# Kernel optimization log

Hardware: AMD Instinct MI355X
Metric: run time of the kernel (lower is better)

Reference implementation:

```python
import jax, jax.numpy as jnp
import numpy as np

BN_EPS = 1e-5

def setup_inputs() -> dict:
    key = jax.random.key(0)
    ks = jax.random.split(key, 7)
    B, D, A = 16384, 768, 51
    s = 1.0 / np.sqrt(D)
    return {
        "x": jax.random.normal(ks[0], (B, D), dtype=jnp.float32),
        "W_embed": jax.random.uniform(ks[1], (D, D), minval=-s, maxval=s, dtype=jnp.float32),
        "b_embed": jax.random.uniform(ks[2], (D,), minval=-s, maxval=s, dtype=jnp.float32),
        "W_attr": jax.random.uniform(ks[3], (A, D), minval=-s, maxval=s, dtype=jnp.float32),  # stacked per-attribute (dim->1) heads
        "b_attr": jax.random.uniform(ks[4], (A,), minval=-s, maxval=s, dtype=jnp.float32),
        "gamma": jnp.ones((A,), dtype=jnp.float32),
        "beta": jnp.zeros((A,), dtype=jnp.float32),
    }

def reference(x, W_embed, b_embed, W_attr, b_attr, gamma, beta):
    # word_embed: Linear(dim, dim)
    h = x @ W_embed.T + b_embed                      # [B, D]
    # fused per-attribute heads: cat of attr_num (dim->1) linears == one (dim->attr_num) matmul
    logits = h @ W_attr.T + b_attr                    # [B, A]
    # BatchNorm1d (training mode: batch statistics, biased variance)
    mean = jnp.mean(logits, axis=0)
    var = jnp.var(logits, axis=0)
    y = (logits - mean) * jax.lax.rsqrt(var + BN_EPS) * gamma + beta
    return y
```

## Files before the change

### kernel.cpp

```cpp
#include <hip/hip_runtime.h>
#include <hip/hip_bf16.h>

typedef _Float16 halfx8 __attribute__((ext_vector_type(8)));
typedef _Float16 halfx4 __attribute__((ext_vector_type(4)));
typedef float floatx4 __attribute__((ext_vector_type(4)));

#define GLOBAL_AS __attribute__((address_space(1)))
#define LDS_AS __attribute__((address_space(3)))

__device__ __forceinline__ void async_copy_16(const _Float16* g, _Float16* l) {
    __builtin_amdgcn_global_load_lds((GLOBAL_AS void*)g, (LDS_AS void*)l, 16, 0, 0);
}

#define PM 16384
#define PD 768
#define PA 51
#define PA_PAD 64


__global__ void convert_all_kernel(const float* __restrict__ x, const float* __restrict__ We,
                                   const float* __restrict__ Wa,
                                   _Float16* __restrict__ x16, _Float16* __restrict__ we16,
                                   _Float16* __restrict__ wa16, float* __restrict__ stats) {
    int b = blockIdx.x, t = threadIdx.x;
    if (b < 12288) {
        int idx = b * 256 + t;
        float4 v = ((const float4*)x)[idx];
        halfx4 h;
        h[0] = (_Float16)v.x; h[1] = (_Float16)v.y; h[2] = (_Float16)v.z; h[3] = (_Float16)v.w;
        *(halfx4*)(x16 + (size_t)idx * 4) = h;
    } else if (b < 12288 + 576) {
        int idx = (b - 12288) * 256 + t;
        float4 v = ((const float4*)We)[idx];
        halfx4 h;
        h[0] = (_Float16)v.x; h[1] = (_Float16)v.y; h[2] = (_Float16)v.z; h[3] = (_Float16)v.w;
        *(halfx4*)(we16 + (size_t)idx * 4) = h;
    } else if (b < 12288 + 624) {
        int j = (b - 12288 - 576) * 256 + t;
        halfx4 h;
        if (j < (PA * PD) / 4) {
            float4 v = ((const float4*)Wa)[j];
            h[0] = (_Float16)v.x; h[1] = (_Float16)v.y; h[2] = (_Float16)v.z; h[3] = (_Float16)v.w;
        } else {
            h[0] = (_Float16)0.f; h[1] = (_Float16)0.f; h[2] = (_Float16)0.f; h[3] = (_Float16)0.f;
        }
        *(halfx4*)(wa16 + (size_t)j * 4) = h;
    } else {
        if (t < 128) stats[t] = 0.f;
    }
}

__global__ __launch_bounds__(256) void gemm1_kernel(
    const _Float16* __restrict__ A,
    const _Float16* __restrict__ B,
    const float* __restrict__ bias,
    _Float16* __restrict__ H)
{
    __shared__ _Float16 As[128 * 64];
    __shared__ _Float16 Bs[128 * 64];
    const int tid = threadIdx.x;
    const int wave = tid >> 6;
    const int lane = tid & 63;
    const int quad = lane >> 4;
    const int l16 = lane & 15;
    const int wm = wave >> 1;
    const int wn = wave & 1;

    int b = blockIdx.x;
    int xcd = b & 7;
    int q = b >> 3;
    int mt = xcd * 16 + (q & 15);
    int nt = q >> 4;
    const int row0 = mt * 128;
    const int col0 = nt * 128;

    const int r_in = lane >> 3;
    const int ksw = ((lane & 7) ^ r_in) * 8;

    const _Float16* Ag = A + (size_t)row0 * PD + ksw;
    const _Float16* Bg = B + (size_t)col0 * PD + ksw;

    floatx4 acc[4][4];
    #pragma unroll
    for (int i = 0; i < 4; ++i)
        #pragma unroll
        for (int j = 0; j < 4; ++j)
            acc[i][j] = (floatx4){0.f, 0.f, 0.f, 0.f};

    for (int kt = 0; kt < PD; kt += 64) {
        #pragma unroll
        for (int j = 0; j < 4; ++j) {
            int i = wave * 4 + j;
            async_copy_16(Ag + (size_t)(i * 8 + r_in) * PD + kt, &As[i * 512]);
            async_copy_16(Bg + (size_t)(i * 8 + r_in) * PD + kt, &Bs[i * 512]);
        }
        __syncthreads();
        #pragma unroll
        for (int ks = 0; ks < 2; ++ks) {
            halfx8 af[4], bf[4];
            #pragma unroll
            for (int mi = 0; mi < 4; ++mi)
                af[mi] = *(const halfx8*)&As[(wm * 64 + mi * 16 + l16) * 64 +
                                             (((ks * 4 + quad) ^ (l16 & 7)) << 3)];
            #pragma unroll
            for (int ni = 0; ni < 4; ++ni)
                bf[ni] = *(const halfx8*)&Bs[(wn * 64 + ni * 16 + l16) * 64 +
                                             (((ks * 4 + quad) ^ (l16 & 7)) << 3)];
            #pragma unroll
            for (int mi = 0; mi < 4; ++mi)
                #pragma unroll
                for (int ni = 0; ni < 4; ++ni)
                    acc[mi][ni] = __builtin_amdgcn_mfma_f32_16x16x32_f16(af[mi], bf[ni], acc[mi][ni], 0, 0, 0);
        }
        __syncthreads();
    }

    #pragma unroll
    for (int ni = 0; ni < 4; ++ni) {
        int col = col0 + wn * 64 + ni * 16 + l16;
        float bv = bias[col];
        #pragma unroll
        for (int mi = 0; mi < 4; ++mi) {
            int rowb = row0 + wm * 64 + mi * 16 + quad * 4;
            #pragma unroll
            for (int r = 0; r < 4; ++r)
                H[(size_t)(rowb + r) * PD + col] = (_Float16)(acc[mi][ni][r] + bv);
        }
    }
}

__global__ __launch_bounds__(256) void gemm2_kernel(
    const _Float16* __restrict__ Hm,
    const _Float16* __restrict__ Wa,
    const float* __restrict__ b_attr,
    float* __restrict__ logits,
    float* __restrict__ stats)
{
    __shared__ _Float16 As[64 * 64];
    __shared__ _Float16 Bs[64 * 64];
    __shared__ float s_sum[64];
    __shared__ float s_ssq[64];
    const int tid = threadIdx.x;
    const int wave = tid >> 6;
    const int lane = tid & 63;
    const int quad = lane >> 4;
    const int l16 = lane & 15;
    const int row0 = blockIdx.x * 64;
    const int r_in = lane >> 3;
    const int ksw = ((lane & 7) ^ r_in) * 8;

    if (tid < 64) { s_sum[tid] = 0.f; s_ssq[tid] = 0.f; }

    const _Float16* Ag = Hm + (size_t)row0 * PD + ksw;
    const _Float16* Bg = Wa + ksw;

    floatx4 acc[4];
    #pragma unroll
    for (int j = 0; j < 4; ++j)
        acc[j] = (floatx4){0.f, 0.f, 0.f, 0.f};

    for (int kt = 0; kt < PD; kt += 64) {
        #pragma unroll
        for (int j = 0; j < 2; ++j) {
            int i = wave * 2 + j;
            async_copy_16(Ag + (size_t)(i * 8 + r_in) * PD + kt, &As[i * 512]);
        }
        #pragma unroll
        for (int j = 0; j < 2; ++j) {
            int i = wave * 2 + j;
            async_copy_16(Bg + (size_t)(i * 8 + r_in) * PD + kt, &Bs[i * 512]);
        }
        __syncthreads();
        #pragma unroll
        for (int ks = 0; ks < 2; ++ks) {
            halfx8 af, bf[4];
            af = *(const halfx8*)&As[(wave * 16 + l16) * 64 +
                                     (((ks * 4 + quad) ^ (l16 & 7)) << 3)];
            #pragma unroll
            for (int ni = 0; ni < 4; ++ni)
                bf[ni] = *(const halfx8*)&Bs[(ni * 16 + l16) * 64 +
                                             (((ks * 4 + quad) ^ (l16 & 7)) << 3)];
            #pragma unroll
            for (int ni = 0; ni < 4; ++ni)
                acc[ni] = __builtin_amdgcn_mfma_f32_16x16x32_f16(af, bf[ni], acc[ni], 0, 0, 0);
        }
        __syncthreads();
    }

    #pragma unroll
    for (int ni = 0; ni < 4; ++ni) {
        int col = ni * 16 + l16;
        if (col < PA) {
            float bv = b_attr[col];
            float ps = 0.f, pss = 0.f;
            int rowb = row0 + wave * 16 + quad * 4;
            #pragma unroll
            for (int r = 0; r < 4; ++r) {
                float v = acc[ni][r] + bv;
                logits[(size_t)(rowb + r) * PA + col] = v;
                ps += v; pss += v * v;
            }
            atomicAdd(&s_sum[col], ps);
            atomicAdd(&s_ssq[col], pss);
        }
    }
    __syncthreads();
    if (tid < PA) {
        atomicAdd(&stats[tid], s_sum[tid]);
        atomicAdd(&stats[64 + tid], s_ssq[tid]);
    }
}

__global__ void bn_finalize_kernel(const float* __restrict__ logits,
                                   const float* __restrict__ stats,
                                   const float* __restrict__ gamma,
                                   const float* __restrict__ beta,
                                   float* __restrict__ out, int total) {
    __shared__ float s_scale[PA];
    __shared__ float s_shift[PA];
    int t = threadIdx.x;
    if (t < PA) {
        const float invB = 1.0f / (float)PM;
        float mean = stats[t] * invB;
        float var = stats[64 + t] * invB - mean * mean;
        float inv = rsqrtf(var + 1e-5f);
        float g = gamma[t] * inv;
        s_scale[t] = g;
        s_shift[t] = beta[t] - mean * g;
    }
    __syncthreads();
    int idx = blockIdx.x * 256 + t;
    if (idx < total) {
        int col = idx % PA;
        out[idx] = logits[idx] * s_scale[col] + s_shift[col];
    }
}

extern "C" void kernel_launch(void* const* d_in, const int* in_sizes, int n_in,
                              void* d_out, int out_size, void* d_ws, size_t ws_size,
                              hipStream_t stream) {
    const float* x       = (const float*)d_in[0];
    const float* W_embed = (const float*)d_in[1];
    const float* b_embed = (const float*)d_in[2];
    const float* W_attr  = (const float*)d_in[3];
    const float* b_attr  = (const float*)d_in[4];
    const float* gamma   = (const float*)d_in[5];
    const float* beta    = (const float*)d_in[6];
    float* out = (float*)d_out;

    char* ws = (char*)d_ws;
    _Float16* x_f16  = (_Float16*)(ws);
    _Float16* we16   = (_Float16*)(ws + 25165824);
    _Float16* wa16   = (_Float16*)(ws + 26345472);
    _Float16* h_f16  = (_Float16*)(ws + 26443776);
    float*    logits = (float*)   (ws + 51609600);
    float*    stats  = (float*)   (ws + 54951936);

    convert_all_kernel<<<12913, 256, 0, stream>>>(x, W_embed, W_attr, x_f16, we16, wa16, stats);
    gemm1_kernel<<<768, 256, 0, stream>>>(x_f16, we16, b_embed, h_f16);
    gemm2_kernel<<<256, 256, 0, stream>>>(h_f16, wa16, b_attr, logits, stats);
    bn_finalize_kernel<<<3264, 256, 0, stream>>>(logits, stats, gamma, beta, out, PM * PA);
}
```

Measured before the change: 153.3 us.

## Fuse fp32-to-fp16 conversion of x into GEMM1 tile loads

GEMM1 now reads the fp32 activations directly, converts them to fp16 in registers and stores the swizzled tile into LDS. The separate conversion pass over the whole 16384x768 input is dropped, which removes a full write and re-read of the fp16 copy. In exchange the A-tile load is now synchronous through registers instead of a direct global-to-LDS copy, and each element is converted once per N tile (6 times). It also adds a launch-bounds occupancy hint and merges two async copy loops in GEMM2.

Result: no change. 155.2 us (+1.3%).

```diff
diff --git a/kernel.cpp b/kernel.cpp
--- a/kernel.cpp
+++ b/kernel.cpp
@@ -18,25 +18,18 @@
 #define PA_PAD 64
 
 
-__global__ void convert_all_kernel(const float* __restrict__ x, const float* __restrict__ We,
-                                   const float* __restrict__ Wa,
-                                   _Float16* __restrict__ x16, _Float16* __restrict__ we16,
-                                   _Float16* __restrict__ wa16, float* __restrict__ stats) {
+__global__ void convert_w_kernel(const float* __restrict__ We, const float* __restrict__ Wa,
+                                 _Float16* __restrict__ we16, _Float16* __restrict__ wa16,
+                                 float* __restrict__ stats) {
     int b = blockIdx.x, t = threadIdx.x;
-    if (b < 12288) {
+    if (b < 576) {
         int idx = b * 256 + t;
-        float4 v = ((const float4*)x)[idx];
-        halfx4 h;
-        h[0] = (_Float16)v.x; h[1] = (_Float16)v.y; h[2] = (_Float16)v.z; h[3] = (_Float16)v.w;
-        *(halfx4*)(x16 + (size_t)idx * 4) = h;
-    } else if (b < 12288 + 576) {
-        int idx = (b - 12288) * 256 + t;
         float4 v = ((const float4*)We)[idx];
         halfx4 h;
         h[0] = (_Float16)v.x; h[1] = (_Float16)v.y; h[2] = (_Float16)v.z; h[3] = (_Float16)v.w;
         *(halfx4*)(we16 + (size_t)idx * 4) = h;
-    } else if (b < 12288 + 624) {
-        int j = (b - 12288 - 576) * 256 + t;
+    } else if (b < 624) {
+        int j = (b - 576) * 256 + t;
         halfx4 h;
         if (j < (PA * PD) / 4) {
             float4 v = ((const float4*)Wa)[j];
@@ -50,8 +43,8 @@
     }
 }
 
-__global__ __launch_bounds__(256) void gemm1_kernel(
-    const _Float16* __restrict__ A,
+__global__ __launch_bounds__(256, 3) void gemm1_kernel(
+    const float* __restrict__ X,
     const _Float16* __restrict__ B,
     const float* __restrict__ bias,
     _Float16* __restrict__ H)
@@ -75,9 +68,10 @@
     const int col0 = nt * 128;
 
     const int r_in = lane >> 3;
-    const int ksw = ((lane & 7) ^ r_in) * 8;
-
-    const _Float16* Ag = A + (size_t)row0 * PD + ksw;
+    const int csw = (lane & 7) ^ r_in;
+    const int ksw = csw * 8;
+
+    const float* Ag = X + (size_t)row0 * PD + ksw;
     const _Float16* Bg = B + (size_t)col0 * PD + ksw;
 
     floatx4 acc[4][4];
@@ -91,7 +85,15 @@
         #pragma unroll
         for (int j = 0; j < 4; ++j) {
             int i = wave * 4 + j;
-            async_copy_16(Ag + (size_t)(i * 8 + r_in) * PD + kt, &As[i * 512]);
+            const float* ap = Ag + (size_t)(i * 8 + r_in) * PD + kt;
+            float4 v0 = *(const float4*)(ap);
+            float4 v1 = *(const float4*)(ap + 4);
+            halfx8 h;
+            h[0] = (_Float16)v0.x; h[1] = (_Float16)v0.y;
+            h[2] = (_Float16)v0.z; h[3] = (_Float16)v0.w;
+            h[4] = (_Float16)v1.x; h[5] = (_Float16)v1.y;
+            h[6] = (_Float16)v1.z; h[7] = (_Float16)v1.w;
+            *(halfx8*)&As[(i * 8 + r_in) * 64 + (lane & 7) * 8] = h;
             async_copy_16(Bg + (size_t)(i * 8 + r_in) * PD + kt, &Bs[i * 512]);
         }
         __syncthreads();
@@ -164,10 +166,6 @@
         for (int j = 0; j < 2; ++j) {
             int i = wave * 2 + j;
             async_copy_16(Ag + (size_t)(i * 8 + r_in) * PD + kt, &As[i * 512]);
-        }
-        #pragma unroll
-        for (int j = 0; j < 2; ++j) {
-            int i = wave * 2 + j;
             async_copy_16(Bg + (size_t)(i * 8 + r_in) * PD + kt, &Bs[i * 512]);
         }
         __syncthreads();
@@ -249,15 +247,14 @@
     float* out = (float*)d_out;
 
     char* ws = (char*)d_ws;
-    _Float16* x_f16  = (_Float16*)(ws);
-    _Float16* we16   = (_Float16*)(ws + 25165824);
-    _Float16* wa16   = (_Float16*)(ws + 26345472);
-    _Float16* h_f16  = (_Float16*)(ws + 26443776);
-    float*    logits = (float*)   (ws + 51609600);
-    float*    stats  = (float*)   (ws + 54951936);
-
-    convert_all_kernel<<<12913, 256, 0, stream>>>(x, W_embed, W_attr, x_f16, we16, wa16, stats);
-    gemm1_kernel<<<768, 256, 0, stream>>>(x_f16, we16, b_embed, h_f16);
+    _Float16* we16   = (_Float16*)(ws);
+    _Float16* wa16   = (_Float16*)(ws + 1179648);
+    _Float16* h_f16  = (_Float16*)(ws + 1277952);
+    float*    logits = (float*)   (ws + 26443776);
+    float*    stats  = (float*)   (ws + 29786112);
+
+    convert_w_kernel<<<625, 256, 0, stream>>>(W_embed, W_attr, we16, wa16, stats);
+    gemm1_kernel<<<768, 256, 0, stream>>>(x, we16, b_embed, h_f16);
     gemm2_kernel<<<256, 256, 0, stream>>>(h_f16, wa16, b_attr, logits, stats);
     bn_finalize_kernel<<<3264, 256, 0, stream>>>(logits, stats, gamma, beta, out, PM * PA);
 }
```

## Fuse both GEMMs so the hidden tile stays in LDS, with atomic split-K logits

Applied to the files above, without the earlier changes.

The first GEMM now keeps its 128x128 fp16 output tile in shared memory and multiplies it right away by the matching 128-column slice of W_attr. Each of the 6 column-tile blocks atomically adds its partial logits into a logits buffer that the convert kernel zero-fills. This removes the 25MB fp16 write and re-read of H and one kernel launch. The cost is 6-way fp32 global atomics on every logit, a separate BN statistics kernel that re-reads logits with shared-memory atomics, and a different summation order.

Result: slower. 264.5 us (+72.5%).

```diff
diff --git a/kernel.cpp b/kernel.cpp
--- a/kernel.cpp
+++ b/kernel.cpp
@@ -21,7 +21,8 @@
 __global__ void convert_all_kernel(const float* __restrict__ x, const float* __restrict__ We,
                                    const float* __restrict__ Wa,
                                    _Float16* __restrict__ x16, _Float16* __restrict__ we16,
-                                   _Float16* __restrict__ wa16, float* __restrict__ stats) {
+                                   _Float16* __restrict__ wa16,
+                                   float* __restrict__ logits, float* __restrict__ stats) {
     int b = blockIdx.x, t = threadIdx.x;
     if (b < 12288) {
         int idx = b * 256 + t;
@@ -45,19 +46,28 @@
             h[0] = (_Float16)0.f; h[1] = (_Float16)0.f; h[2] = (_Float16)0.f; h[3] = (_Float16)0.f;
         }
         *(halfx4*)(wa16 + (size_t)j * 4) = h;
+    } else if (b < 12288 + 624 + 816) {
+        int idx4 = (b - 12288 - 624) * 256 + t;
+        ((float4*)logits)[idx4] = (float4){0.f, 0.f, 0.f, 0.f};
     } else {
         if (t < 128) stats[t] = 0.f;
     }
 }
 
-__global__ __launch_bounds__(256) void gemm1_kernel(
+__global__ __launch_bounds__(256, 3) void megagemm_kernel(
     const _Float16* __restrict__ A,
     const _Float16* __restrict__ B,
-    const float* __restrict__ bias,
-    _Float16* __restrict__ H)
+    const _Float16* __restrict__ Wa,
+    const float* __restrict__ b_embed,
+    const float* __restrict__ b_attr,
+    float* __restrict__ logits)
 {
-    __shared__ _Float16 As[128 * 64];
-    __shared__ _Float16 Bs[128 * 64];
+    __shared__ __align__(16) char smem[49152];
+    _Float16* As  = (_Float16*)smem;
+    _Float16* Bs  = (_Float16*)(smem + 16384);
+    _Float16* Was = (_Float16*)(smem + 32768);
+    _Float16* Hs  = (_Float16*)smem;
+
     const int tid = threadIdx.x;
     const int wave = tid >> 6;
     const int lane = tid & 63;
@@ -77,6 +87,18 @@
     const int r_in = lane >> 3;
     const int ksw = ((lane & 7) ^ r_in) * 8;
 
+    {
+        int rl = lane >> 4;
+        int cl = lane & 15;
+        #pragma unroll
+        for (int j = 0; j < 4; ++j) {
+            int i = wave * 4 + j;
+            int row = i * 4 + rl;
+            int c = cl ^ (row & 7);
+            async_copy_16(Wa + (size_t)row * PD + col0 + c * 8, &Was[i * 512]);
+        }
+    }
+
     const _Float16* Ag = A + (size_t)row0 * PD + ksw;
     const _Float16* Bg = B + (size_t)col0 * PD + ksw;
 
@@ -117,97 +139,85 @@
 
     #pragma unroll
     for (int ni = 0; ni < 4; ++ni) {
-        int col = col0 + wn * 64 + ni * 16 + l16;
-        float bv = bias[col];
+        int C = wn * 64 + ni * 16 + l16;
+        float bv = b_embed[col0 + C];
+        int cc = C >> 3;
+        int co = C & 7;
         #pragma unroll
         for (int mi = 0; mi < 4; ++mi) {
-            int rowb = row0 + wm * 64 + mi * 16 + quad * 4;
-            #pragma unroll
-            for (int r = 0; r < 4; ++r)
-                H[(size_t)(rowb + r) * PD + col] = (_Float16)(acc[mi][ni][r] + bv);
-        }
-    }
-}
-
-__global__ __launch_bounds__(256) void gemm2_kernel(
-    const _Float16* __restrict__ Hm,
-    const _Float16* __restrict__ Wa,
-    const float* __restrict__ b_attr,
-    float* __restrict__ logits,
-    float* __restrict__ stats)
-{
-    __shared__ _Float16 As[64 * 64];
-    __shared__ _Float16 Bs[64 * 64];
-    __shared__ float s_sum[64];
-    __shared__ float s_ssq[64];
-    const int tid = threadIdx.x;
-    const int wave = tid >> 6;
-    const int lane = tid & 63;
-    const int quad = lane >> 4;
-    const int l16 = lane & 15;
-    const int row0 = blockIdx.x * 64;
-    const int r_in = lane >> 3;
-    const int ksw = ((lane & 7) ^ r_in) * 8;
-
-    if (tid < 64) { s_sum[tid] = 0.f; s_ssq[tid] = 0.f; }
-
-    const _Float16* Ag = Hm + (size_t)row0 * PD + ksw;
-    const _Float16* Bg = Wa + ksw;
-
-    floatx4 acc[4];
-    #pragma unroll
-    for (int j = 0; j < 4; ++j)
-        acc[j] = (floatx4){0.f, 0.f, 0.f, 0.f};
-
-    for (int kt = 0; kt < PD; kt += 64) {
-        #pragma unroll
-        for (int j = 0; j < 2; ++j) {
-            int i = wave * 2 + j;
-            async_copy_16(Ag + (size_t)(i * 8 + r_in) * PD + kt, &As[i * 512]);
-        }
-        #pragma unroll
-        for (int j = 0; j < 2; ++j) {
-            int i = wave * 2 + j;
-            async_copy_16(Bg + (size_t)(i * 8 + r_in) * PD + kt, &Bs[i * 512]);
-        }
-        __syncthreads();
-        #pragma unroll
-        for (int ks = 0; ks < 2; ++ks) {
-            halfx8 af, bf[4];
-            af = *(const halfx8*)&As[(wave * 16 + l16) * 64 +
-                                     (((ks * 4 + quad) ^ (l16 & 7)) << 3)];
-            #pragma unroll
-            for (int ni = 0; ni < 4; ++ni)
-                bf[ni] = *(const halfx8*)&Bs[(ni * 16 + l16) * 64 +
-                                             (((ks * 4 + quad) ^ (l16 & 7)) << 3)];
-            #pragma unroll
-            for (int ni = 0; ni < 4; ++ni)
-                acc[ni] = __builtin_amdgcn_mfma_f32_16x16x32_f16(af, bf[ni], acc[ni], 0, 0, 0);
-        }
-        __syncthreads();
-    }
-
-    #pragma unroll
-    for (int ni = 0; ni < 4; ++ni) {
-        int col = ni * 16 + l16;
-        if (col < PA) {
-            float bv = b_attr[col];
-            float ps = 0.f, pss = 0.f;
-            int rowb = row0 + wave * 16 + quad * 4;
             #pragma unroll
             for (int r = 0; r < 4; ++r) {
-                float v = acc[ni][r] + bv;
-                logits[(size_t)(rowb + r) * PA + col] = v;
-                ps += v; pss += v * v;
+                int R = wm * 64 + mi * 16 + quad * 4 + r;
+                Hs[R * 128 + ((cc ^ (R & 7)) << 3) + co] = (_Float16)(acc[mi][ni][r] + bv);
             }
-            atomicAdd(&s_sum[col], ps);
-            atomicAdd(&s_ssq[col], pss);
-        }
-    }
-    __syncthreads();
-    if (tid < PA) {
-        atomicAdd(&stats[tid], s_sum[tid]);
-        atomicAdd(&stats[64 + tid], s_ssq[tid]);
+        }
+    }
+    __syncthreads();
+
+    floatx4 acc2[4][2];
+    #pragma unroll
+    for (int i = 0; i < 4; ++i)
+        #pragma unroll
+        for (int j = 0; j < 2; ++j)
+            acc2[i][j] = (floatx4){0.f, 0.f, 0.f, 0.f};
+
+    #pragma unroll
+    for (int ks2 = 0; ks2 < 4; ++ks2) {
+        halfx8 afr[4], bfr[2];
+        #pragma unroll
+        for (int mf = 0; mf < 4; ++mf)
+            afr[mf] = *(const halfx8*)&Was[(mf * 16 + l16) * 128 +
+                                           (((ks2 * 4 + quad) ^ (l16 & 7)) << 3)];
+        #pragma unroll
+        for (int nf = 0; nf < 2; ++nf)
+            bfr[nf] = *(const halfx8*)&Hs[(wave * 32 + nf * 16 + l16) * 128 +
+                                          (((ks2 * 4 + quad) ^ (l16 & 7)) << 3)];
+        #pragma unroll
+        for (int mf = 0; mf < 4; ++mf)
+            #pragma unroll
+            for (int nf = 0; nf < 2; ++nf)
+                acc2[mf][nf] = __builtin_amdgcn_mfma_f32_16x16x32_f16(afr[mf], bfr[nf], acc2[mf][nf], 0, 0, 0);
+    }
+
+    const bool add_bias = (nt == 0);
+    #pragma unroll
+    for (int mf = 0; mf < 4; ++mf) {
+        #pragma unroll
+        for (int nf = 0; nf < 2; ++nf) {
+            int grow = row0 + wave * 32 + nf * 16 + l16;
+            #pragma unroll
+            for (int r = 0; r < 4; ++r) {
+                int attr = mf * 16 + quad * 4 + r;
+                if (attr < PA) {
+                    float v = acc2[mf][nf][r];
+                    if (add_bias) v += b_attr[attr];
+                    atomicAdd(&logits[(size_t)grow * PA + attr], v);
+                }
+            }
+        }
+    }
+}
+
+__global__ void bn_stats_kernel(const float* __restrict__ logits, float* __restrict__ stats) {
+    __shared__ float s_sum[PA];
+    __shared__ float s_ssq[PA];
+    int t = threadIdx.x;
+    if (t < PA) { s_sum[t] = 0.f; s_ssq[t] = 0.f; }
+    __syncthreads();
+    int idx4 = blockIdx.x * 256 + t;
+    float4 v = ((const float4*)logits)[idx4];
+    float vals[4] = {v.x, v.y, v.z, v.w};
+    int base = idx4 * 4;
+    #pragma unroll
+    for (int j = 0; j < 4; ++j) {
+        int col = (base + j) % PA;
+        atomicAdd(&s_sum[col], vals[j]);
+        atomicAdd(&s_ssq[col], vals[j] * vals[j]);
+    }
+    __syncthreads();
+    if (t < PA) {
+        atomicAdd(&stats[t], s_sum[t]);
+        atomicAdd(&stats[64 + t], s_ssq[t]);
     }
 }
 
@@ -252,12 +262,11 @@
     _Float16* x_f16  = (_Float16*)(ws);
     _Float16* we16   = (_Float16*)(ws + 25165824);
     _Float16* wa16   = (_Float16*)(ws + 26345472);
-    _Float16* h_f16  = (_Float16*)(ws + 26443776);
-    float*    logits = (float*)   (ws + 51609600);
-    float*    stats  = (float*)   (ws + 54951936);
-
-    convert_all_kernel<<<12913, 256, 0, stream>>>(x, W_embed, W_attr, x_f16, we16, wa16, stats);
-    gemm1_kernel<<<768, 256, 0, stream>>>(x_f16, we16, b_embed, h_f16);
-    gemm2_kernel<<<256, 256, 0, stream>>>(h_f16, wa16, b_attr, logits, stats);
+    float*    logits = (float*)   (ws + 26443776);
+    float*    stats  = (float*)   (ws + 29786112);
+
+    convert_all_kernel<<<13729, 256, 0, stream>>>(x, W_embed, W_attr, x_f16, we16, wa16, logits, stats);
+    megagemm_kernel<<<768, 256, 0, stream>>>(x_f16, we16, wa16, b_embed, b_attr, logits);
+    bn_stats_kernel<<<816, 256, 0, stream>>>(logits, stats);
     bn_finalize_kernel<<<3264, 256, 0, stream>>>(logits, stats, gamma, beta, out, PM * PA);
 }
```
